# Kernel optimization log

Hardware: AMD Instinct MI355X
Metric: run time of the kernel (lower is better)

Reference implementation:

```python
import jax, jax.numpy as jnp
import numpy as np

HIDDEN = 1024
NUM_QUBITS = 16
QUBIT_DIM = 64  # HIDDEN == NUM_QUBITS * QUBIT_DIM
LN_EPS = 1e-6   # flax nn.LayerNorm default


def setup_inputs() -> dict:
    key = jax.random.key(0)
    k_x, k_w = jax.random.split(key)
    B, S = 4, 4096
    x = jax.random.normal(k_x, (B, S, HIDDEN), dtype=jnp.float32)
    # Learned params (flax defaults: LN scale=ones, bias=zeros; Dense lecun_normal kernel, zero bias)
    ln_scale = jnp.ones((HIDDEN,), dtype=jnp.float32)
    ln_bias = jnp.zeros((HIDDEN,), dtype=jnp.float32)
    dense_w = jax.random.normal(k_w, (HIDDEN, HIDDEN), dtype=jnp.float32) * (1.0 / np.sqrt(HIDDEN))
    dense_b = jnp.zeros((HIDDEN,), dtype=jnp.float32)
    return {"x": x, "ln_scale": ln_scale, "ln_bias": ln_bias,
            "dense_w": dense_w, "dense_b": dense_b}


def reference(x, ln_scale, ln_bias, dense_w, dense_b):
    B, S, H = x.shape
    # input_preparation: LayerNorm over last axis, then reshape (B,S,Q,D)
    mean = jnp.mean(x, axis=-1, keepdims=True)
    var = jnp.mean(jnp.square(x - mean), axis=-1, keepdims=True)
    h = (x - mean) * jax.lax.rsqrt(var + LN_EPS) * ln_scale + ln_bias
    h = h.reshape(B, S, NUM_QUBITS, QUBIT_DIM)
    # quantum_forward (default jax backend): sin*cos, FFT along qubit axis, real part
    h = jnp.sin(h) * jnp.cos(h)
    h = jnp.real(jnp.fft.fft(h.astype(jnp.complex64), axis=-2))
    # post_process: restore (B,S,H) then Dense(hidden_size)
    h = h.reshape(B, S, H)
    return jnp.einsum('bsh,hk->bsk', h, dense_w) + dense_b
```

## Files before the change

kernel.cpp:

```cpp
#include <hip/hip_runtime.h>
#include <hip/hip_bf16.h>

#define HID 1024
#define MROWS 16384

typedef __bf16 bf16;
typedef __bf16 bf16x8 __attribute__((ext_vector_type(8)));
typedef __bf16 bf16x4 __attribute__((ext_vector_type(4)));
typedef float f32x4 __attribute__((ext_vector_type(4)));

#define MFMA(va, vb, vc) __builtin_amdgcn_mfma_f32_16x16x32_bf16(va, vb, vc, 0, 0, 0)

__global__ __launch_bounds__(256) void wt_k(const float* __restrict__ W,
                                            bf16* __restrict__ Wt) {
    __shared__ float Wl[1024][17];
    const int tid = threadIdx.x;
    const int n0 = blockIdx.x * 16;

    {
        int r = tid >> 2, nq = tid & 3;
#pragma unroll
        for (int p = 0; p < 16; ++p) {
            int k = p * 64 + r;
            float4 v = *(const float4*)&W[(size_t)k * HID + n0 + nq * 4];
            Wl[k][nq * 4 + 0] = v.x; Wl[k][nq * 4 + 1] = v.y;
            Wl[k][nq * 4 + 2] = v.z; Wl[k][nq * 4 + 3] = v.w;
        }
    }
    __syncthreads();

    const float ct[16] = {
        1.0f,  0.92387953f,  0.70710678f,  0.38268343f,
        0.0f, -0.38268343f, -0.70710678f, -0.92387953f,
       -1.0f, -0.92387953f, -0.70710678f, -0.38268343f,
        0.0f,  0.38268343f,  0.70710678f,  0.92387953f};

    const int d = tid & 63, ng = tid >> 6;
#pragma unroll
    for (int nn = 0; nn < 4; ++nn) {
        int n = ng * 4 + nn;
        float wv[16];
#pragma unroll
        for (int qp = 0; qp < 16; ++qp) wv[qp] = Wl[qp * 64 + d][n];
#pragma unroll
        for (int q = 0; q < 16; ++q) {
            float acc = 0.0f;
#pragma unroll
            for (int qp = 0; qp < 16; ++qp) acc += wv[qp] * ct[(q * qp) & 15];
            Wt[(size_t)(n0 + n) * HID + q * 64 + d] = (bf16)acc;
        }
    }
}

__global__ __launch_bounds__(256) void prep_k(const float* __restrict__ x,
                                              const float* __restrict__ gamma,
                                              const float* __restrict__ beta,
                                              bf16* __restrict__ A) {
    int row = blockIdx.x;
    int t = threadIdx.x;
    const float4* xr = (const float4*)(x + (size_t)row * HID);
    float4 v = xr[t];

    float s  = v.x + v.y + v.z + v.w;
    float ss = v.x * v.x + v.y * v.y + v.z * v.z + v.w * v.w;
#pragma unroll
    for (int off = 32; off; off >>= 1) {
        s  += __shfl_down(s, off);
        ss += __shfl_down(ss, off);
    }
    __shared__ float red[8];
    int wv = t >> 6, ln = t & 63;
    if (ln == 0) { red[wv] = s; red[4 + wv] = ss; }
    __syncthreads();
    float Sm = red[0] + red[1] + red[2] + red[3];
    float Ss = red[4] + red[5] + red[6] + red[7];
    float mean = Sm * (1.0f / HID);
    float var  = Ss * (1.0f / HID) - mean * mean;
    float rstd = rsqrtf(var + 1e-6f);

    float4 g = ((const float4*)gamma)[t];
    float4 b = ((const float4*)beta)[t];

    float h0 = (v.x - mean) * rstd * g.x + b.x;
    float h1 = (v.y - mean) * rstd * g.y + b.y;
    float h2 = (v.z - mean) * rstd * g.z + b.z;
    float h3 = (v.w - mean) * rstd * g.w + b.w;

    bf16x4 o;
    o[0] = (bf16)(0.5f * __sinf(2.0f * h0));
    o[1] = (bf16)(0.5f * __sinf(2.0f * h1));
    o[2] = (bf16)(0.5f * __sinf(2.0f * h2));
    o[3] = (bf16)(0.5f * __sinf(2.0f * h3));
    ((bf16x4*)(A + (size_t)row * HID))[t] = o;
}

#define BM 256
#define BN 256
#define BK 64
#define NT (HID / BK)

__global__ __launch_bounds__(512, 2) void gemm_k(const bf16* __restrict__ A,
                                                 const bf16* __restrict__ Bt,
                                                 const float* __restrict__ bias,
                                                 float* __restrict__ C) {
    __shared__ __attribute__((aligned(16))) char lds[131072];

    const int tid = threadIdx.x;
    const int w = tid >> 6, ln = tid & 63;
    const int wm = w >> 2, wn = w & 3;
    const int fr = ln & 15, fq = ln >> 4;

    int orig = blockIdx.x;
    int wg = (orig & 7) * 32 + (orig >> 3);
    int bm = wg >> 2, bn = wg & 3;

    const bf16* Ab = A + (size_t)bm * BM * HID;
    const bf16* Bb = Bt + (size_t)bn * BN * HID;

    auto stage = [&](int buf, int mat, int R0, int kt) {
        const char* gsrc = (const char*)(mat ? Bb : Ab);
        char* base = lds + (((buf << 1) | mat) << 15) + (R0 << 7);
        const int kb = kt << 7;
#pragma unroll
        for (int l = 0; l < 2; ++l) {
            int c = (l << 9) + tid;
            int lr = c >> 3;
            int colB = ((c & 7) ^ (lr & 7)) << 4;
            const char* g = gsrc + (size_t)(R0 + lr) * (HID * 2) + kb + colB;
            __builtin_amdgcn_global_load_lds(
                (const __attribute__((address_space(1))) void*)g,
                (__attribute__((address_space(3))) void*)(base + (((l << 9) + (w << 6)) << 4)),
                16, 0, 0);
        }
    };

    auto readA = [&](int buf, int i, int ks) -> bf16x8 {
        int r = ((i * 2 + wm) << 4) + fr;
        int off = (r << 7) + (ks << 6) + (fq << 4);
        off ^= (fr & 7) << 4;
        return *(const bf16x8*)(lds + ((buf << 1) << 15) + off);
    };
    auto readB = [&](int buf, int j, int ks) -> bf16x8 {
        int r = ((j * 4 + wn) << 4) + fr;
        int off = (r << 7) + (ks << 6) + (fq << 4);
        off ^= (fr & 7) << 4;
        return *(const bf16x8*)(lds + (((buf << 1) | 1) << 15) + off);
    };

    f32x4 acc[8][4];
#pragma unroll
    for (int i = 0; i < 8; ++i)
#pragma unroll
        for (int j = 0; j < 4; ++j) acc[i][j] = (f32x4){0.f, 0.f, 0.f, 0.f};

    stage(0, 1, 0, 0);
    stage(0, 0, 128, 0);
    stage(0, 0, 0, 0);
    stage(0, 1, 128, 0);
    stage(1, 1, 0, 1);
    stage(1, 0, 128, 1);
    asm volatile("s_waitcnt vmcnt(4)" ::: "memory");
    __builtin_amdgcn_s_barrier();

    bf16x8 a[8][2], b[4][2];

#pragma unroll 1
    for (int t = 0; t < NT; ++t) {
        const int cur = t & 1, nxt = cur ^ 1;

#pragma unroll
        for (int i = 0; i < 4; ++i) { a[i][0] = readA(cur, i, 0); a[i][1] = readA(cur, i, 1); }
#pragma unroll
        for (int j = 0; j < 2; ++j) { b[j][0] = readB(cur, j, 0); b[j][1] = readB(cur, j, 1); }
        if (t + 1 < NT) stage(nxt, 0, 0, t + 1);
        __builtin_amdgcn_s_barrier();
        asm volatile("s_waitcnt lgkmcnt(0)" ::: "memory");
        __builtin_amdgcn_sched_barrier(0);
        __builtin_amdgcn_s_setprio(1);
#pragma unroll
        for (int i = 0; i < 4; ++i)
#pragma unroll
            for (int j = 0; j < 2; ++j) {
                acc[i][j] = MFMA(a[i][0], b[j][0], acc[i][j]);
                acc[i][j] = MFMA(a[i][1], b[j][1], acc[i][j]);
            }
        __builtin_amdgcn_s_setprio(0);
        __builtin_amdgcn_s_barrier();

#pragma unroll
        for (int i = 4; i < 8; ++i) { a[i][0] = readA(cur, i, 0); a[i][1] = readA(cur, i, 1); }
        if (t + 1 < NT) stage(nxt, 1, 128, t + 1);
        __builtin_amdgcn_s_barrier();
        asm volatile("s_waitcnt lgkmcnt(0)" ::: "memory");
        __builtin_amdgcn_sched_barrier(0);
        __builtin_amdgcn_s_setprio(1);
#pragma unroll
        for (int i = 4; i < 8; ++i)
#pragma unroll
            for (int j = 0; j < 2; ++j) {
                acc[i][j] = MFMA(a[i][0], b[j][0], acc[i][j]);
                acc[i][j] = MFMA(a[i][1], b[j][1], acc[i][j]);
            }
        __builtin_amdgcn_s_setprio(0);
        __builtin_amdgcn_s_barrier();

#pragma unroll
        for (int j = 2; j < 4; ++j) { b[j][0] = readB(cur, j, 0); b[j][1] = readB(cur, j, 1); }
        if (t + 2 < NT) stage(cur, 1, 0, t + 2);
        __builtin_amdgcn_s_barrier();
        asm volatile("s_waitcnt lgkmcnt(0)" ::: "memory");
        __builtin_amdgcn_sched_barrier(0);
        __builtin_amdgcn_s_setprio(1);
#pragma unroll
        for (int i = 4; i < 8; ++i)
#pragma unroll
            for (int j = 2; j < 4; ++j) {
                acc[i][j] = MFMA(a[i][0], b[j][0], acc[i][j]);
                acc[i][j] = MFMA(a[i][1], b[j][1], acc[i][j]);
            }
        __builtin_amdgcn_s_setprio(0);
        __builtin_amdgcn_s_barrier();

        if (t + 2 < NT) stage(cur, 0, 128, t + 2);
        __builtin_amdgcn_s_barrier();
        __builtin_amdgcn_s_setprio(1);
#pragma unroll
        for (int i = 0; i < 4; ++i)
#pragma unroll
            for (int j = 2; j < 4; ++j) {
                acc[i][j] = MFMA(a[i][0], b[j][0], acc[i][j]);
                acc[i][j] = MFMA(a[i][1], b[j][1], acc[i][j]);
            }
        __builtin_amdgcn_s_setprio(0);
        if (t + 2 < NT) {
            asm volatile("s_waitcnt vmcnt(4)" ::: "memory");
        } else if (t + 1 < NT) {
            asm volatile("s_waitcnt vmcnt(0)" ::: "memory");
        }
        __builtin_amdgcn_sched_barrier(0);
        __builtin_amdgcn_s_barrier();
    }

#pragma unroll
    for (int j = 0; j < 4; ++j) {
        int col = bn * BN + ((j * 4 + wn) << 4) + fr;
        float bv = bias[col];
#pragma unroll
        for (int i = 0; i < 8; ++i) {
            int row0 = bm * BM + ((i * 2 + wm) << 4) + (fq << 2);
#pragma unroll
            for (int jj = 0; jj < 4; ++jj)
                C[(size_t)(row0 + jj) * HID + col] = acc[i][j][jj] + bv;
        }
    }
}

extern "C" void kernel_launch(void* const* d_in, const int* in_sizes, int n_in,
                              void* d_out, int out_size, void* d_ws, size_t ws_size,
                              hipStream_t stream) {
    const float* x   = (const float*)d_in[0];
    const float* lng = (const float*)d_in[1];
    const float* lnb = (const float*)d_in[2];
    const float* W   = (const float*)d_in[3];
    const float* db  = (const float*)d_in[4];
    float* out = (float*)d_out;

    bf16* A  = (bf16*)d_ws;
    bf16* Wt = (bf16*)((char*)d_ws + (size_t)MROWS * HID * 2);

    wt_k<<<HID / 16, 256, 0, stream>>>(W, Wt);
    prep_k<<<MROWS, 256, 0, stream>>>(x, lng, lnb, A);
    gemm_k<<<(MROWS / BM) * (HID / BN), 512, 0, stream>>>(A, Wt, db, out);
}
```

Before: 68.93 us.

## Fuse weight transform, LayerNorm prep and GEMM into one cooperative kernel

Merges the three launches (weight DFT transform, LayerNorm+sin prep, bf16 GEMM) into a single cooperative kernel of 256 blocks. Each block first transforms four weight columns and normalizes 64 rows with one wave per row, then a grid-wide sync separates this from the GEMM phase. This removes two kernel launches and the gaps between them. In exchange it adds a grid barrier, relies on all 256 blocks being co-resident, and the weight transform now reads W with strided uncoalesced global loads instead of staging it through LDS.

```diff
diff --git a/kernel.cpp b/kernel.cpp
--- a/kernel.cpp
+++ b/kernel.cpp
@@ -1,5 +1,8 @@
 #include <hip/hip_runtime.h>
 #include <hip/hip_bf16.h>
+#include <hip/hip_cooperative_groups.h>
+
+namespace cg = cooperative_groups;
 
 #define HID 1024
 #define MROWS 16384
@@ -11,111 +14,97 @@
 
 #define MFMA(va, vb, vc) __builtin_amdgcn_mfma_f32_16x16x32_bf16(va, vb, vc, 0, 0, 0)
 
-__global__ __launch_bounds__(256) void wt_k(const float* __restrict__ W,
-                                            bf16* __restrict__ Wt) {
-    __shared__ float Wl[1024][17];
-    const int tid = threadIdx.x;
-    const int n0 = blockIdx.x * 16;
-
-    {
-        int r = tid >> 2, nq = tid & 3;
-#pragma unroll
-        for (int p = 0; p < 16; ++p) {
-            int k = p * 64 + r;
-            float4 v = *(const float4*)&W[(size_t)k * HID + n0 + nq * 4];
-            Wl[k][nq * 4 + 0] = v.x; Wl[k][nq * 4 + 1] = v.y;
-            Wl[k][nq * 4 + 2] = v.z; Wl[k][nq * 4 + 3] = v.w;
-        }
-    }
-    __syncthreads();
-
-    const float ct[16] = {
-        1.0f,  0.92387953f,  0.70710678f,  0.38268343f,
-        0.0f, -0.38268343f, -0.70710678f, -0.92387953f,
-       -1.0f, -0.92387953f, -0.70710678f, -0.38268343f,
-        0.0f,  0.38268343f,  0.70710678f,  0.92387953f};
-
-    const int d = tid & 63, ng = tid >> 6;
-#pragma unroll
-    for (int nn = 0; nn < 4; ++nn) {
-        int n = ng * 4 + nn;
-        float wv[16];
-#pragma unroll
-        for (int qp = 0; qp < 16; ++qp) wv[qp] = Wl[qp * 64 + d][n];
-#pragma unroll
-        for (int q = 0; q < 16; ++q) {
-            float acc = 0.0f;
-#pragma unroll
-            for (int qp = 0; qp < 16; ++qp) acc += wv[qp] * ct[(q * qp) & 15];
-            Wt[(size_t)(n0 + n) * HID + q * 64 + d] = (bf16)acc;
-        }
-    }
-}
-
-__global__ __launch_bounds__(256) void prep_k(const float* __restrict__ x,
-                                              const float* __restrict__ gamma,
-                                              const float* __restrict__ beta,
-                                              bf16* __restrict__ A) {
-    int row = blockIdx.x;
-    int t = threadIdx.x;
-    const float4* xr = (const float4*)(x + (size_t)row * HID);
-    float4 v = xr[t];
-
-    float s  = v.x + v.y + v.z + v.w;
-    float ss = v.x * v.x + v.y * v.y + v.z * v.z + v.w * v.w;
-#pragma unroll
-    for (int off = 32; off; off >>= 1) {
-        s  += __shfl_down(s, off);
-        ss += __shfl_down(ss, off);
-    }
-    __shared__ float red[8];
-    int wv = t >> 6, ln = t & 63;
-    if (ln == 0) { red[wv] = s; red[4 + wv] = ss; }
-    __syncthreads();
-    float Sm = red[0] + red[1] + red[2] + red[3];
-    float Ss = red[4] + red[5] + red[6] + red[7];
-    float mean = Sm * (1.0f / HID);
-    float var  = Ss * (1.0f / HID) - mean * mean;
-    float rstd = rsqrtf(var + 1e-6f);
-
-    float4 g = ((const float4*)gamma)[t];
-    float4 b = ((const float4*)beta)[t];
-
-    float h0 = (v.x - mean) * rstd * g.x + b.x;
-    float h1 = (v.y - mean) * rstd * g.y + b.y;
-    float h2 = (v.z - mean) * rstd * g.z + b.z;
-    float h3 = (v.w - mean) * rstd * g.w + b.w;
-
-    bf16x4 o;
-    o[0] = (bf16)(0.5f * __sinf(2.0f * h0));
-    o[1] = (bf16)(0.5f * __sinf(2.0f * h1));
-    o[2] = (bf16)(0.5f * __sinf(2.0f * h2));
-    o[3] = (bf16)(0.5f * __sinf(2.0f * h3));
-    ((bf16x4*)(A + (size_t)row * HID))[t] = o;
-}
-
 #define BM 256
 #define BN 256
 #define BK 64
 #define NT (HID / BK)
 
-__global__ __launch_bounds__(512, 2) void gemm_k(const bf16* __restrict__ A,
-                                                 const bf16* __restrict__ Bt,
-                                                 const float* __restrict__ bias,
-                                                 float* __restrict__ C) {
+__global__ __launch_bounds__(512, 2) void fused_k(const float* __restrict__ x,
+                                                  const float* __restrict__ gamma,
+                                                  const float* __restrict__ beta,
+                                                  const float* __restrict__ W,
+                                                  const float* __restrict__ bias,
+                                                  bf16* __restrict__ A,
+                                                  bf16* __restrict__ Wt,
+                                                  float* __restrict__ C) {
     __shared__ __attribute__((aligned(16))) char lds[131072];
 
     const int tid = threadIdx.x;
     const int w = tid >> 6, ln = tid & 63;
+    const int orig = blockIdx.x;
+    const int wg = (orig & 7) * 32 + (orig >> 3);
+
+    if (tid < 256) {
+        const float ct[16] = {
+            1.0f,  0.92387953f,  0.70710678f,  0.38268343f,
+            0.0f, -0.38268343f, -0.70710678f, -0.92387953f,
+           -1.0f, -0.92387953f, -0.70710678f, -0.38268343f,
+            0.0f,  0.38268343f,  0.70710678f,  0.92387953f};
+        int n = orig * 4 + (tid >> 6);
+        int d = tid & 63;
+        float wv[16];
+#pragma unroll
+        for (int qp = 0; qp < 16; ++qp)
+            wv[qp] = W[(size_t)(qp * 64 + d) * HID + n];
+#pragma unroll
+        for (int q = 0; q < 16; ++q) {
+            float acc = 0.0f;
+#pragma unroll
+            for (int qp = 0; qp < 16; ++qp) acc += wv[qp] * ct[(q * qp) & 15];
+            Wt[(size_t)n * HID + q * 64 + d] = (bf16)acc;
+        }
+    }
+
+    {
+        float4 g4[4], bb4[4];
+#pragma unroll
+        for (int c = 0; c < 4; ++c) {
+            g4[c]  = *(const float4*)&gamma[c * 256 + ln * 4];
+            bb4[c] = *(const float4*)&beta[c * 256 + ln * 4];
+        }
+#pragma unroll 1
+        for (int it = 0; it < 8; ++it) {
+            int row = wg * 64 + it * 8 + w;
+            const float* xr = x + (size_t)row * HID;
+            float4 v[4];
+            float s = 0.f, ss = 0.f;
+#pragma unroll
+            for (int c = 0; c < 4; ++c) {
+                v[c] = *(const float4*)&xr[c * 256 + ln * 4];
+                s  += v[c].x + v[c].y + v[c].z + v[c].w;
+                ss += v[c].x * v[c].x + v[c].y * v[c].y + v[c].z * v[c].z + v[c].w * v[c].w;
+            }
+#pragma unroll
+            for (int off = 32; off; off >>= 1) {
+                s  += __shfl_xor(s, off);
+                ss += __shfl_xor(ss, off);
+            }
+            float mean = s * (1.0f / HID);
+            float rstd = rsqrtf(ss * (1.0f / HID) - mean * mean + 1e-6f);
+#pragma unroll
+            for (int c = 0; c < 4; ++c) {
+                float h0 = (v[c].x - mean) * rstd * g4[c].x + bb4[c].x;
+                float h1 = (v[c].y - mean) * rstd * g4[c].y + bb4[c].y;
+                float h2 = (v[c].z - mean) * rstd * g4[c].z + bb4[c].z;
+                float h3 = (v[c].w - mean) * rstd * g4[c].w + bb4[c].w;
+                bf16x4 o;
+                o[0] = (bf16)(0.5f * __sinf(2.0f * h0));
+                o[1] = (bf16)(0.5f * __sinf(2.0f * h1));
+                o[2] = (bf16)(0.5f * __sinf(2.0f * h2));
+                o[3] = (bf16)(0.5f * __sinf(2.0f * h3));
+                *(bf16x4*)&A[(size_t)row * HID + c * 256 + ln * 4] = o;
+            }
+        }
+    }
+
+    cg::this_grid().sync();
+
     const int wm = w >> 2, wn = w & 3;
     const int fr = ln & 15, fq = ln >> 4;
-
-    int orig = blockIdx.x;
-    int wg = (orig & 7) * 32 + (orig >> 3);
-    int bm = wg >> 2, bn = wg & 3;
+    const int bm = wg >> 2, bn = wg & 3;
 
     const bf16* Ab = A + (size_t)bm * BM * HID;
-    const bf16* Bb = Bt + (size_t)bn * BN * HID;
+    const bf16* Bb = Wt + (size_t)bn * BN * HID;
 
     auto stage = [&](int buf, int mat, int R0, int kt) {
         const char* gsrc = (const char*)(mat ? Bb : Ab);
@@ -268,7 +257,7 @@
     bf16* A  = (bf16*)d_ws;
     bf16* Wt = (bf16*)((char*)d_ws + (size_t)MROWS * HID * 2);
 
-    wt_k<<<HID / 16, 256, 0, stream>>>(W, Wt);
-    prep_k<<<MROWS, 256, 0, stream>>>(x, lng, lnb, A);
-    gemm_k<<<(MROWS / BM) * (HID / BN), 512, 0, stream>>>(A, Wt, db, out);
+    void* args[] = {(void*)&x, (void*)&lng, (void*)&lnb, (void*)&W, (void*)&db,
+                    (void*)&A, (void*)&Wt, (void*)&out};
+    hipLaunchCooperativeKernel((void*)fused_k, dim3(256), dim3(512), args, 0, stream);
 }
```

Result: slower. 109.7 us (+59.1%).
